# Kernel optimization log

Hardware: AMD Instinct MI355X
Metric: run time of the kernel (lower is better)

The kernel has to match this reference:

```python
import jax, jax.numpy as jnp
import numpy as np


def _fft_upsample2(x):
    """Ideal (sinc) 2x upsample via FFT zero-padding, with Nyquist-bin splitting.
    x: [B, C, H, W] real -> [B, C, 2H, 2W] real."""
    H, W = x.shape[-2], x.shape[-1]
    hh, hw = H // 2, W // 2
    # shifted spectrum: index i along length-H axis <-> frequency i - H/2
    X = jnp.fft.fftshift(jnp.fft.fft2(x), axes=(-2, -1))
    Y = jnp.zeros(x.shape[:-2] + (2 * H, 2 * W), X.dtype)
    Y = Y.at[..., hh:hh + H, hw:hw + W].set(X)
    # split Nyquist row -H/2 (index hh) into +/-H/2 (indices hh and hh+H), each half
    Y = Y.at[..., hh, :].multiply(0.5)
    Y = Y.at[..., hh + H, :].set(Y[..., hh, :])
    # same for Nyquist column
    Y = Y.at[..., :, hw].multiply(0.5)
    Y = Y.at[..., :, hw + W].set(Y[..., :, hw])
    y = jnp.fft.ifft2(jnp.fft.ifftshift(Y, axes=(-2, -1))).real
    return (y * 4.0).astype(x.dtype)  # up**2 amplitude correction


def _lpf_rect_1d(N, cutoff):
    # create_lpf_rect from alias_free_convnets: ideal rect LPF in frequency
    cl = int(N * cutoff) // 2
    ch = N - cl
    rect = np.ones(N, dtype=np.float32)
    rect[cl + 1:ch] = 0.0
    if N % 4 == 0:  # half-weight on the exact cutoff (Nyquist-of-subband) bins
        rect[cl] = 0.5
        rect[ch] = 0.5
    return rect


def _lpf_rfft(x, cutoff=0.5):
    """Ideal low-pass via rfft2 with rectangular separable mask."""
    H, W = x.shape[-2], x.shape[-1]
    rect_h = _lpf_rect_1d(H, cutoff)
    rect_w = _lpf_rect_1d(W, cutoff)
    mask = jnp.asarray(rect_h[:, None] * rect_w[None, :W // 2 + 1])
    X = jnp.fft.rfft2(x) * mask
    return jnp.fft.irfft2(X, s=(H, W)).astype(x.dtype)


def setup_inputs() -> dict:
    key = jax.random.key(0)
    x = jax.random.normal(key, (8, 256, 64, 64), dtype=jnp.float32)
    return {"x": x}


def reference(x):
    u = _fft_upsample2(x)          # [B, C, 2H, 2W]
    a = jax.nn.silu(u)
    f = _lpf_rfft(a, cutoff=0.5)   # [B, C, 2H, 2W]
    return f[:, :, ::2, ::2]       # [B, C, H, W]
```

## Files before the change

### kernel.cpp

```cpp
#include <hip/hip_runtime.h>
#include <math.h>

#define TPB 256

typedef _Float16 f16x8 __attribute__((ext_vector_type(8)));
typedef float    f32x4 __attribute__((ext_vector_type(4)));

#define MFMA16(A, B, C) __builtin_amdgcn_mfma_f32_16x16x32_f16((A), (B), (C), 0, 0, 0)


__device__ __forceinline__ int sw64(int r, int c) {
  return (r << 6) + (c & 7) + ((((c >> 3) ^ r) & 7) << 3);
}
__device__ __forceinline__ int sw128(int r, int c) {
  return (r << 7) + (c & 7) + ((((c >> 3) ^ (r & 7))) << 3);
}

__device__ __forceinline__ void store4h(_Float16* p, float a0, float a1, float a2, float a3) {
  float2 q;
  q.x = __builtin_bit_cast(float, __builtin_amdgcn_cvt_pkrtz(a0, a1));
  q.y = __builtin_bit_cast(float, __builtin_amdgcn_cvt_pkrtz(a2, a3));
  *(float2*)p = q;
}

__global__ __launch_bounds__(TPB, 3) void warped_mfma(const float* __restrict__ xin,
                                                      float* __restrict__ outp, int nimg) {
  __shared__ __attribute__((aligned(16))) _Float16 bufA[128 * 128];
  __shared__ __attribute__((aligned(16))) _Float16 bufB[128 * 64];
  __shared__ float k1d[128];

  _Float16* const buf0 = bufA;
  _Float16* const buf2 = bufA;
  _Float16* const buf1 = bufB;
  _Float16* const buf3 = bufB;

  const int tid = threadIdx.x;
  const int lane = tid & 63;
  const int w  = tid >> 6;
  const int wk = w >> 1;
  const int wd = w & 1;
  const int lq = lane >> 4;
  const int ln = lane & 15;

  if (tid < 128) {
    const int d = tid;
    float s = 1.0f + ((d & 1) ? 0.0f : ((d & 2) ? -1.0f : 1.0f));
    for (int f = 1; f <= 31; ++f) {
      int r = (f * d) & 127;
      s += 2.0f * __cosf((float)r * 0.04908738521234052f );
    }
    k1d[d] = s * (1.0f / 64.0f);
  }
  __syncthreads();

  f16x8 AK[4][2];
#pragma unroll
  for (int t = 0; t < 4; ++t)
#pragma unroll
    for (int ks = 0; ks < 2; ++ks) {
      const int a = (wk * 4 + t) * 16 + ln;
      f16x8 f;
#pragma unroll
      for (int j = 0; j < 8; ++j) {
        int k = ks * 32 + lq * 8 + j;
        f[j] = (_Float16)k1d[(a - 2 * k) & 127];
      }
      AK[t][ks] = f;
    }
  f16x8 BT[2][4];
#pragma unroll
  for (int t = 0; t < 2; ++t)
#pragma unroll
    for (int ks = 0; ks < 4; ++ks) {
      const int c = (wk * 2 + t) * 16 + ln;
      f16x8 f;
#pragma unroll
      for (int j = 0; j < 8; ++j) {
        int k = ks * 32 + lq * 8 + j;
        f[j] = (_Float16)k1d[(k - 2 * c) & 127];
      }
      BT[t][ks] = f;
    }

  const f32x4 vzero = {0.0f, 0.0f, 0.0f, 0.0f};

  for (int img = blockIdx.x; img < nimg; img += gridDim.x) {
    const float* __restrict__ x = xin + (size_t)img * 4096;
    float* __restrict__ out     = outp + (size_t)img * 4096;

#pragma unroll
    for (int rep = 0; rep < 4; ++rep) {
      int idx = rep * 256 + tid;
      float4 v = ((const float4*)x)[idx];
      int i = idx >> 4, j0 = (idx & 15) << 2;
      store4h(buf0 + sw64(i, j0), v.x, v.y, v.z, v.w);
    }
    __syncthreads();

    {
      f32x4 acc[2][4];
#pragma unroll
      for (int mtl = 0; mtl < 2; ++mtl)
#pragma unroll
        for (int ntl = 0; ntl < 4; ++ntl) acc[mtl][ntl] = vzero;
#pragma unroll
      for (int ks = 0; ks < 2; ++ks) {
        f16x8 Ad[2];
#pragma unroll
        for (int mtl = 0; mtl < 2; ++mtl)
          Ad[mtl] = *(const f16x8*)(buf0 + sw64((wd * 2 + mtl) * 16 + ln, ks * 32 + lq * 8));
#pragma unroll
        for (int mtl = 0; mtl < 2; ++mtl)
#pragma unroll
          for (int ntl = 0; ntl < 4; ++ntl)
            acc[mtl][ntl] = MFMA16(Ad[mtl], AK[ntl][ks], acc[mtl][ntl]);
      }
#pragma unroll
      for (int mtl = 0; mtl < 2; ++mtl)
#pragma unroll
        for (int ntl = 0; ntl < 4; ++ntl) {
          int n0 = (wk * 4 + ntl) * 16, m0 = (wd * 2 + mtl) * 16;
          f32x4 a = acc[mtl][ntl];
          store4h(buf1 + sw64(n0 + ln, m0 + lq * 4), a[0], a[1], a[2], a[3]);
        }
    }
    __syncthreads();

#pragma unroll
    for (int nh = 0; nh < 2; ++nh) {
      f32x4 acc[4][2];
#pragma unroll
      for (int mtl = 0; mtl < 4; ++mtl)
#pragma unroll
        for (int ntl = 0; ntl < 2; ++ntl) acc[mtl][ntl] = vzero;
#pragma unroll
      for (int ks = 0; ks < 2; ++ks) {
        f16x8 Bd[2];
#pragma unroll
        for (int ntl = 0; ntl < 2; ++ntl)
          Bd[ntl] = *(const f16x8*)(buf1 +
                                    sw64((wd * 4 + nh * 2 + ntl) * 16 + ln, ks * 32 + lq * 8));
#pragma unroll
        for (int mtl = 0; mtl < 4; ++mtl)
#pragma unroll
          for (int ntl = 0; ntl < 2; ++ntl)
            acc[mtl][ntl] = MFMA16(AK[mtl][ks], Bd[ntl], acc[mtl][ntl]);
      }
#pragma unroll
      for (int mtl = 0; mtl < 4; ++mtl)
#pragma unroll
        for (int ntl = 0; ntl < 2; ++ntl) {
          int n0 = (wd * 4 + nh * 2 + ntl) * 16, m0 = (wk * 4 + mtl) * 16;
          float s[4];
#pragma unroll
          for (int r = 0; r < 4; ++r) {
            float u = acc[mtl][ntl][r];
            s[r] = u * __builtin_amdgcn_rcpf(1.0f + __expf(-u));
          }
          store4h(buf2 + sw128(n0 + ln, m0 + lq * 4), s[0], s[1], s[2], s[3]);
        }
    }
    __syncthreads();

    {
      f32x4 acc[4][2];
#pragma unroll
      for (int mtl = 0; mtl < 4; ++mtl)
#pragma unroll
        for (int ntl = 0; ntl < 2; ++ntl) acc[mtl][ntl] = vzero;
#pragma unroll
      for (int ks = 0; ks < 4; ++ks) {
        f16x8 Ad[4];
#pragma unroll
        for (int mtl = 0; mtl < 4; ++mtl)
          Ad[mtl] = *(const f16x8*)(buf2 + sw128((wd * 4 + mtl) * 16 + ln, ks * 32 + lq * 8));
#pragma unroll
        for (int mtl = 0; mtl < 4; ++mtl)
#pragma unroll
          for (int ntl = 0; ntl < 2; ++ntl)
            acc[mtl][ntl] = MFMA16(Ad[mtl], BT[ntl][ks], acc[mtl][ntl]);
      }
#pragma unroll
      for (int mtl = 0; mtl < 4; ++mtl)
#pragma unroll
        for (int ntl = 0; ntl < 2; ++ntl) {
          int n0 = (wk * 2 + ntl) * 16, m0 = (wd * 4 + mtl) * 16;
          f32x4 a = acc[mtl][ntl];
          store4h(buf3 + sw128(n0 + ln, m0 + lq * 4), a[0], a[1], a[2], a[3]);
        }
    }
    __syncthreads();

    {
      f32x4 acc[2][2];
#pragma unroll
      for (int mtl = 0; mtl < 2; ++mtl)
#pragma unroll
        for (int ntl = 0; ntl < 2; ++ntl) acc[mtl][ntl] = vzero;
#pragma unroll
      for (int ks = 0; ks < 4; ++ks) {
        f16x8 Ad[2];
#pragma unroll
        for (int mtl = 0; mtl < 2; ++mtl)
          Ad[mtl] = *(const f16x8*)(buf3 + sw128((wd * 2 + mtl) * 16 + ln, ks * 32 + lq * 8));
#pragma unroll
        for (int mtl = 0; mtl < 2; ++mtl)
#pragma unroll
          for (int ntl = 0; ntl < 2; ++ntl)
            acc[mtl][ntl] = MFMA16(Ad[mtl], BT[ntl][ks], acc[mtl][ntl]);
      }
#pragma unroll
      for (int mtl = 0; mtl < 2; ++mtl)
#pragma unroll
        for (int ntl = 0; ntl < 2; ++ntl) {
          int n0 = (wk * 2 + ntl) * 16, m0 = (wd * 2 + mtl) * 16;
#pragma unroll
          for (int r = 0; r < 4; ++r)
            out[(m0 + lq * 4 + r) * 64 + n0 + ln] = 0.25f * acc[mtl][ntl][r];
        }
    }
  }
}

extern "C" void kernel_launch(void* const* d_in, const int* in_sizes, int n_in,
                              void* d_out, int out_size, void* d_ws, size_t ws_size,
                              hipStream_t stream) {
  const float* x = (const float*)d_in[0];
  float* out = (float*)d_out;
  const int nimg = in_sizes[0] / 4096;
  const int grid = (nimg + 1) / 2;
  warped_mfma<<<dim3(grid), dim3(TPB), 0, stream>>>(x, out, nimg);
}
```

Before: 116.1 us.

## Prefetch next image into registers and stage output through LDS for coalesced stores

Loads the next image's input tile into registers while the current image is processed, hiding global load latency behind the MFMA stages. Final results are written to a padded fp32 LDS buffer and then stored to global memory as coalesced float4 writes instead of strided scalar writes. This adds an extra barrier and 16 live registers, which may pressure occupancy.

```diff
diff --git a/kernel.cpp b/kernel.cpp
--- a/kernel.cpp
+++ b/kernel.cpp
@@ -25,12 +25,15 @@
 
 __global__ __launch_bounds__(TPB, 3) void warped_mfma(const float* __restrict__ xin,
                                                       float* __restrict__ outp, int nimg) {
+  constexpr int SZ = 68;
+
   __shared__ __attribute__((aligned(16))) _Float16 bufA[128 * 128];
   __shared__ __attribute__((aligned(16))) _Float16 bufB[128 * 64];
   __shared__ float k1d[128];
 
   _Float16* const buf0 = bufA;
   _Float16* const buf2 = bufA;
+  float*    const buf4 = (float*)(bufA + 4096);
   _Float16* const buf1 = bufB;
   _Float16* const buf3 = bufB;
 
@@ -84,16 +87,29 @@
 
   const f32x4 vzero = {0.0f, 0.0f, 0.0f, 0.0f};
 
+  float4 pf[4];
+  {
+    const float4* xp = (const float4*)(xin + (size_t)blockIdx.x * 4096);
+#pragma unroll
+    for (int rep = 0; rep < 4; ++rep) pf[rep] = xp[rep * 256 + tid];
+  }
+
   for (int img = blockIdx.x; img < nimg; img += gridDim.x) {
-    const float* __restrict__ x = xin + (size_t)img * 4096;
-    float* __restrict__ out     = outp + (size_t)img * 4096;
+    float* __restrict__ out = outp + (size_t)img * 4096;
 
 #pragma unroll
     for (int rep = 0; rep < 4; ++rep) {
       int idx = rep * 256 + tid;
-      float4 v = ((const float4*)x)[idx];
       int i = idx >> 4, j0 = (idx & 15) << 2;
-      store4h(buf0 + sw64(i, j0), v.x, v.y, v.z, v.w);
+      store4h(buf0 + sw64(i, j0), pf[rep].x, pf[rep].y, pf[rep].z, pf[rep].w);
+    }
+    {
+      int img2 = img + gridDim.x;
+      if (img2 < nimg) {
+        const float4* xp = (const float4*)(xin + (size_t)img2 * 4096);
+#pragma unroll
+        for (int rep = 0; rep < 4; ++rep) pf[rep] = xp[rep * 256 + tid];
+      }
     }
     __syncthreads();
 
@@ -216,8 +232,17 @@
           int n0 = (wk * 2 + ntl) * 16, m0 = (wd * 2 + mtl) * 16;
 #pragma unroll
           for (int r = 0; r < 4; ++r)
-            out[(m0 + lq * 4 + r) * 64 + n0 + ln] = 0.25f * acc[mtl][ntl][r];
-        }
+            buf4[(m0 + lq * 4 + r) * SZ + n0 + ln] = 0.25f * acc[mtl][ntl][r];
+        }
+    }
+    __syncthreads();
+
+#pragma unroll
+    for (int rep = 0; rep < 4; ++rep) {
+      int a = (tid >> 4) + rep * 16;
+      int b0 = (tid & 15) << 2;
+      float4 o = *(const float4*)(buf4 + a * SZ + b0);
+      ((float4*)out)[(a * 64 + b0) >> 2] = o;
     }
   }
 }
```

After: 116.6 us. Within noise of the previous version (+0.4%).
